# Optimization experiments

Hardware: AMD Instinct MI355X
Metric: run time of the kernel (lower is better)

The kernel has to match this reference:

```python
import jax, jax.numpy as jnp
import numpy as np

IN_FEATS = 64
ONSET = 0.8
CUTOFF = 1.0
N_NODES = 100000
N_EDGES = 1600000


def smooth_cutoff(d):
    # 1 below onset, 0 above cutoff, smooth cosine ramp in between
    x = (d - ONSET) / (CUTOFF - ONSET)
    ramp = 0.5 * (jnp.cos(jnp.pi * jnp.clip(x, 0.0, 1.0)) + 1.0)
    return jnp.where(d <= ONSET, 1.0, jnp.where(d >= CUTOFF, 0.0, ramp))


def setup_inputs() -> dict:
    key = jax.random.key(0)
    ks = jax.random.split(key, 8)
    h = jax.random.normal(ks[0], (N_NODES, IN_FEATS), dtype=jnp.float32)
    dist = jax.random.uniform(ks[1], (N_EDGES,), dtype=jnp.float32)
    W1 = jax.random.normal(ks[2], (IN_FEATS, IN_FEATS), dtype=jnp.float32) / jnp.sqrt(IN_FEATS)
    b1 = jnp.zeros((IN_FEATS,), dtype=jnp.float32)
    W2 = jax.random.normal(ks[3], (IN_FEATS, IN_FEATS), dtype=jnp.float32) / jnp.sqrt(IN_FEATS)
    b2 = jnp.zeros((IN_FEATS,), dtype=jnp.float32)
    src_idx = jax.random.randint(ks[4], (N_EDGES,), 0, N_NODES, dtype=jnp.int64 if jax.config.jax_enable_x64 else jnp.int32).astype(jnp.int32)
    dst_idx = jax.random.randint(ks[5], (N_EDGES,), 0, N_NODES, dtype=jnp.int32)
    return {"h": h, "dist": dist, "W1": W1, "b1": b1, "W2": W2, "b2": b2,
            "src_idx": src_idx, "dst_idx": dst_idx}


def reference(h, dist, W1, b1, W2, b2, src_idx, dst_idx):
    gamma = jnp.float32(IN_FEATS / (CUTOFF - 0.0))  # in_feats / (range hi - lo)
    muk = jnp.linspace(0.0, CUTOFF, IN_FEATS, dtype=jnp.float32)  # [K]
    # per-edge RBF basis: [E, K]
    rbf = jnp.exp(-gamma * (dist[:, None] - muk[None, :]) ** 2)
    fcut = smooth_cutoff(dist)[:, None]  # [E, 1]
    msg = h[src_idx] * rbf * fcut  # gather src feats, [E, K]
    agg = jax.ops.segment_sum(msg, dst_idx, num_segments=N_NODES)  # [N, K]
    # MLP: Linear -> softplus -> Linear
    hid = jax.nn.softplus(agg @ W1 + b1)
    out = hid @ W2 + b2
    return out
```

## Files before the change

kernel.cpp:

```cpp
#include <hip/hip_runtime.h>
#include <hip/hip_fp16.h>
#include <math.h>

#define IN_FEATS 64
#define N_NODES 100000
#define N_EDGES 1600000
#define BSHIFT 7
#define NPB 128
#define NBUCK ((N_NODES + NPB - 1) / NPB)
#define CAP 4088
#define PCHUNK 8192
#define PGRID ((N_EDGES + PCHUNK - 1) / PCHUNK)
#define NGRP (N_NODES / 16)

#define KSCALE 9.6089785f

typedef __attribute__((ext_vector_type(8))) short short8_t;
typedef __attribute__((ext_vector_type(4))) float f32x4_t;

#define MFMA16(a, b, c) __builtin_amdgcn_mfma_f32_16x16x32_bf16(a, b, c, 0, 0, 0)

__device__ __forceinline__ unsigned short bf16_rne(float x) {
    unsigned u = __float_as_uint(x);
    unsigned r = u + 0x7FFFu + ((u >> 16) & 1u);
    return (unsigned short)(r >> 16);
}

__device__ __forceinline__ short8_t u4_to_s8(uint4 v) {
    union { uint4 u; short8_t s; } cv; cv.u = v; return cv.s;
}

__device__ __forceinline__ void split8(float4 a, float4 b,
                                       short8_t* hi, short8_t* lo) {
    short8_t h, l;
#define SP(I, X) { unsigned short hu = bf16_rne(X); \
        float hf = __uint_as_float((unsigned)hu << 16); \
        unsigned short lu = bf16_rne((X) - hf); \
        h[I] = (short)hu; l[I] = (short)lu; }
    SP(0, a.x) SP(1, a.y) SP(2, a.z) SP(3, a.w)
    SP(4, b.x) SP(5, b.y) SP(6, b.z) SP(7, b.w)
#undef SP
    *hi = h; *lo = l;
}

__device__ __forceinline__ float edge_coef(float d, float mu) {
    float t = d - mu;
    float rbf = __expf(-64.0f * t * t);
    float x  = (d - 0.8f) * 5.0f;
    float xc = fminf(fmaxf(x, 0.0f), 1.0f);
    float ramp = 0.5f * (__cosf(3.14159265358979323846f * xc) + 1.0f);
    float fc = (d <= 0.8f) ? 1.0f : ((d >= 1.0f) ? 0.0f : ramp);
    return rbf * fc;
}

__device__ __forceinline__ float cutoff_fc(float d) {
    float x  = (d - 0.8f) * 5.0f;
    float xc = fminf(fmaxf(x, 0.0f), 1.0f);
    float ramp = 0.5f * (__cosf(3.14159265358979323846f * xc) + 1.0f);
    return (d <= 0.8f) ? 1.0f : ((d >= 1.0f) ? 0.0f : ramp);
}

__global__ __launch_bounds__(256) void init_kernel(int* __restrict__ bcursor,
                                                   int* __restrict__ offs,
                                                   const float* __restrict__ W1,
                                                   const float* __restrict__ W2,
                                                   uint4* __restrict__ wfrag,
                                                   const float* __restrict__ h,
                                                   unsigned short* __restrict__ hb) {
    int i = blockIdx.x * 256 + threadIdx.x;
    if (i < NBUCK) bcursor[i] = i * CAP;
    if (i == 0) offs[N_NODES] = N_EDGES;
    if (i < 2048) {
        int lane  = i & 63;
        int tile  = (i >> 6) & 7;
        int hl    = (i >> 9) & 1;
        int layer = (i >> 10) & 1;
        const float* W = layer ? W2 : W1;
        int kbase = (tile >> 2) * 32 + (lane >> 4) * 8;
        int j     = (tile & 3) * 16 + (lane & 15);
        unsigned p[4];
        #pragma unroll
        for (int e = 0; e < 8; e += 2) {
            float x0 = W[(kbase + e) * 64 + j];
            float x1 = W[(kbase + e + 1) * 64 + j];
            unsigned short u0, u1;
            if (hl == 0) {
                u0 = bf16_rne(x0);
                u1 = bf16_rne(x1);
            } else {
                unsigned short h0 = bf16_rne(x0);
                unsigned short h1 = bf16_rne(x1);
                u0 = bf16_rne(x0 - __uint_as_float((unsigned)h0 << 16));
                u1 = bf16_rne(x1 - __uint_as_float((unsigned)h1 << 16));
            }
            p[e >> 1] = (unsigned)u0 | ((unsigned)u1 << 16);
        }
        wfrag[i] = make_uint4(p[0], p[1], p[2], p[3]);
    }
    if (i < N_NODES * 8) {
        const float4* p = (const float4*)(h + (size_t)i * 8);
        float4 a = p[0], b = p[1];
        unsigned u0 = (unsigned)bf16_rne(a.x) | ((unsigned)bf16_rne(a.y) << 16);
        unsigned u1 = (unsigned)bf16_rne(a.z) | ((unsigned)bf16_rne(a.w) << 16);
        unsigned u2 = (unsigned)bf16_rne(b.x) | ((unsigned)bf16_rne(b.y) << 16);
        unsigned u3 = (unsigned)bf16_rne(b.z) | ((unsigned)bf16_rne(b.w) << 16);
        *(uint4*)(hb + (size_t)i * 8) = make_uint4(u0, u1, u2, u3);
    }
}

__global__ __launch_bounds__(1024) void partition_kernel(const int* __restrict__ dst,
                                                         const int* __restrict__ src,
                                                         const float* __restrict__ dist,
                                                         int* __restrict__ bcursor,
                                                         int2* __restrict__ brec) {
    __shared__ int hist[NBUCK];
    __shared__ int base_[NBUCK];
    int tid = threadIdx.x;
    for (int i = tid; i < NBUCK; i += 1024) hist[i] = 0;
    __syncthreads();

    int e0 = blockIdx.x * PCHUNK;
    int e1 = min(e0 + PCHUNK, N_EDGES);

    for (int t = e0 + tid; t < e1; t += 1024)
        atomicAdd(&hist[dst[t] >> BSHIFT], 1);
    __syncthreads();

    for (int i = tid; i < NBUCK; i += 1024) {
        int hv = hist[i];
        if (hv) base_[i] = atomicAdd(&bcursor[i], hv);
        hist[i] = 0;
    }
    __syncthreads();

    for (int t = e0 + tid; t < e1; t += 1024) {
        int d  = dst[t];
        int b  = d >> BSHIFT;
        int r  = atomicAdd(&hist[b], 1);
        float dv = dist[t];
        float fc = cutoff_fc(dv);
        float lfc = (fc > 0.0f) ? __log2f(fc) : -512.0f;
        unsigned dq = (unsigned)(fminf(fmaxf(dv, 0.0f), 1.0f) * 65535.0f + 0.5f);
        unsigned hf = (unsigned)__half_as_ushort(__float2half(lfc));
        int2 rec;
        rec.x = src[t] | ((d & (NPB - 1)) << 17);
        rec.y = (int)((hf << 16) | dq);
        brec[(size_t)base_[b] + r] = rec;
    }
}

__global__ __launch_bounds__(1024) void bscan_kernel(const int* __restrict__ bcursor,
                                                     int* __restrict__ boffs) {
    __shared__ int lds[1024];
    int tid = threadIdx.x;
    int v = (tid < NBUCK) ? (bcursor[tid] - tid * CAP) : 0;
    lds[tid] = v;
    __syncthreads();
    for (int off = 1; off < 1024; off <<= 1) {
        int x = (tid >= off) ? lds[tid - off] : 0;
        __syncthreads();
        lds[tid] += x;
        __syncthreads();
    }
    if (tid < NBUCK) boffs[tid] = lds[tid] - v;
    if (tid == 0) boffs[NBUCK] = N_EDGES;
}

__global__ __launch_bounds__(256) void node_sort_kernel(const int2* __restrict__ brec,
                                                        const int* __restrict__ boffs,
                                                        int2* __restrict__ rec_sorted,
                                                        int* __restrict__ offs) {
    __shared__ int cntL[NPB];
    __shared__ int scanL[NPB];
    __shared__ int curL[NPB];
    __shared__ int2 stage[CAP];

    int b   = blockIdx.x;
    int tid = threadIdx.x;
    int beg = boffs[b];
    int cnt = boffs[b + 1] - beg;
    size_t pbase = (size_t)b * CAP;
    int node0 = b << BSHIFT;

    for (int i = tid; i < NPB; i += 256) cntL[i] = 0;
    __syncthreads();

    for (int t = tid; t < cnt; t += 256) {
        int2 r = brec[pbase + t];
        stage[t] = r;
        atomicAdd(&cntL[(r.x >> 17) & (NPB - 1)], 1);
    }
    __syncthreads();

    if (tid < NPB) scanL[tid] = cntL[tid];
    __syncthreads();
    for (int off = 1; off < NPB; off <<= 1) {
        int x = 0;
        if (tid < NPB && tid >= off) x = scanL[tid - off];
        __syncthreads();
        if (tid < NPB) scanL[tid] += x;
        __syncthreads();
    }
    if (tid < NPB) {
        int excl = scanL[tid] - cntL[tid];
        curL[tid] = excl;
        int node = node0 + tid;
        if (node < N_NODES) offs[node] = beg + excl;
    }
    __syncthreads();

    for (int t = tid; t < cnt; t += 256) {
        int2 r = stage[t];
        int dl = (r.x >> 17) & (NPB - 1);
        int p  = atomicAdd(&curL[dl], 1);
        rec_sorted[(size_t)beg + p] = r;
    }
}

__global__ __launch_bounds__(256) void agg_bf16_kernel(
    const unsigned short* __restrict__ hb,
    const int* __restrict__ offs,
    const int2* __restrict__ rec_sorted,
    float* __restrict__ out)
{
    int w    = threadIdx.x >> 6;
    int lane = threadIdx.x & 63;
    int node = blockIdx.x * 4 + w;
    if (node >= N_NODES) return;

    int beg = __builtin_amdgcn_readfirstlane(offs[node]);
    int end = __builtin_amdgcn_readfirstlane(offs[node + 1]);
    float muK = (float)lane * (KSCALE / 63.0f);
    float acc0 = 0.0f, acc1 = 0.0f;

#define REC(J, ACC) { \
        int2 r_ = rec_sorted[(size_t)(J)]; \
        int rx_ = __builtin_amdgcn_readfirstlane(r_.x); \
        unsigned ry_ = (unsigned)__builtin_amdgcn_readfirstlane(r_.y); \
        unsigned hvu_ = (unsigned)hb[((size_t)(rx_ & 0x1FFFF) << 6) + lane]; \
        float hv_ = __uint_as_float(hvu_ << 16); \
        float dqf_ = (float)(ry_ & 0xFFFFu); \
        float lfc_ = __half2float(__ushort_as_half((unsigned short)(ry_ >> 16))); \
        float t_  = fmaf(dqf_, (KSCALE / 65535.0f), -muK); \
        float a_  = fmaf(-t_, t_, lfc_); \
        ACC = fmaf(hv_, exp2f(a_), ACC); }

    int i = beg;
    int main_end = beg + ((end - beg) & ~7);
    for (; i < main_end; i += 8) {
        REC(i + 0, acc0) REC(i + 1, acc1) REC(i + 2, acc0) REC(i + 3, acc1)
        REC(i + 4, acc0) REC(i + 5, acc1) REC(i + 6, acc0) REC(i + 7, acc1)
    }
    for (; i < end; ++i) { REC(i, acc0) }
#undef REC

    out[(size_t)node * 64 + lane] = acc0 + acc1;
}

__global__ __launch_bounds__(256) void agg_kernel(
    const float* __restrict__ h,
    const int* __restrict__ offs,
    const int2* __restrict__ rec_sorted,
    float* __restrict__ out)
{
    int w    = threadIdx.x >> 6;
    int lane = threadIdx.x & 63;
    int node = blockIdx.x * 4 + w;
    if (node >= N_NODES) return;

    int beg = __builtin_amdgcn_readfirstlane(offs[node]);
    int end = __builtin_amdgcn_readfirstlane(offs[node + 1]);
    float muK = (float)lane * (KSCALE / 63.0f);
    float acc0 = 0.0f, acc1 = 0.0f;

#define REC(J, ACC) { \
        int2 r_ = rec_sorted[(size_t)(J)]; \
        int rx_ = __builtin_amdgcn_readfirstlane(r_.x); \
        unsigned ry_ = (unsigned)__builtin_amdgcn_readfirstlane(r_.y); \
        float hv_ = h[((size_t)(rx_ & 0x1FFFF) << 6) + lane]; \
        float dqf_ = (float)(ry_ & 0xFFFFu); \
        float lfc_ = __half2float(__ushort_as_half((unsigned short)(ry_ >> 16))); \
        float t_  = fmaf(dqf_, (KSCALE / 65535.0f), -muK); \
        float a_  = fmaf(-t_, t_, lfc_); \
        ACC = fmaf(hv_, exp2f(a_), ACC); }

    int i = beg;
    int main_end = beg + ((end - beg) & ~7);
    for (; i < main_end; i += 8) {
        REC(i + 0, acc0) REC(i + 1, acc1) REC(i + 2, acc0) REC(i + 3, acc1)
        REC(i + 4, acc0) REC(i + 5, acc1) REC(i + 6, acc0) REC(i + 7, acc1)
    }
    for (; i < end; ++i) { REC(i, acc0) }
#undef REC

    out[(size_t)node * 64 + lane] = acc0 + acc1;
}

__global__ __launch_bounds__(256) void mlp_kernel(
    float* __restrict__ io, const uint4* __restrict__ wfrag,
    const float* __restrict__ b1, const float* __restrict__ b2)
{
    __shared__ float hidL[4][16][68];

    int tid  = threadIdx.x;
    int lane = tid & 63;
    int wv   = tid >> 6;
    int grp  = blockIdx.x * 4 + wv;
    if (grp >= NGRP) return;
    int node0 = grp * 16;
    int lrow = lane & 15, lk = lane >> 4;

    const float* arow = io + (size_t)(node0 + lrow) * 64 + lk * 8;
    float4 t0 = *(const float4*)(arow);
    float4 t1 = *(const float4*)(arow + 4);
    float4 t2 = *(const float4*)(arow + 32);
    float4 t3 = *(const float4*)(arow + 36);
    short8_t Ah0, Al0, Ah1, Al1;
    split8(t0, t1, &Ah0, &Al0);
    split8(t2, t3, &Ah1, &Al1);

    f32x4_t acc[4];
    #pragma unroll
    for (int n = 0; n < 4; ++n) {
        float b = b1[n * 16 + lrow];
        acc[n] = (f32x4_t){b, b, b, b};
    }
    #pragma unroll
    for (int n = 0; n < 4; ++n) {
        short8_t wh0 = u4_to_s8(wfrag[(n) * 64 + lane]);
        short8_t wh1 = u4_to_s8(wfrag[(4 + n) * 64 + lane]);
        short8_t wl0 = u4_to_s8(wfrag[512 + n * 64 + lane]);
        short8_t wl1 = u4_to_s8(wfrag[512 + (4 + n) * 64 + lane]);
        f32x4_t c = acc[n];
        c = MFMA16(Ah0, wh0, c);
        c = MFMA16(Ah1, wh1, c);
        c = MFMA16(Ah0, wl0, c);
        c = MFMA16(Ah1, wl1, c);
        c = MFMA16(Al0, wh0, c);
        c = MFMA16(Al1, wh1, c);
        acc[n] = c;
    }

    #pragma unroll
    for (int n = 0; n < 4; ++n) {
        #pragma unroll
        for (int r = 0; r < 4; ++r) {
            float v = acc[n][r];
            float e = exp2f(v * 1.44269504089f);
            float sp = 0.69314718056f * __log2f(1.0f + e);
            v = (v > 20.0f) ? v : sp;
            hidL[wv][lk * 4 + r][n * 16 + lrow] = v;
        }
    }
    __threadfence_block();

    const float* hrow = &hidL[wv][lrow][lk * 8];
    float4 h0 = *(const float4*)(hrow);
    float4 h1 = *(const float4*)(hrow + 4);
    float4 h2 = *(const float4*)(hrow + 32);
    float4 h3 = *(const float4*)(hrow + 36);
    short8_t Bh0, Bl0, Bh1, Bl1;
    split8(h0, h1, &Bh0, &Bl0);
    split8(h2, h3, &Bh1, &Bl1);

    f32x4_t oac[4];
    #pragma unroll
    for (int n = 0; n < 4; ++n) {
        float b = b2[n * 16 + lrow];
        oac[n] = (f32x4_t){b, b, b, b};
    }
    #pragma unroll
    for (int n = 0; n < 4; ++n) {
        short8_t wh0 = u4_to_s8(wfrag[1024 + n * 64 + lane]);
        short8_t wh1 = u4_to_s8(wfrag[1024 + (4 + n) * 64 + lane]);
        short8_t wl0 = u4_to_s8(wfrag[1536 + n * 64 + lane]);
        short8_t wl1 = u4_to_s8(wfrag[1536 + (4 + n) * 64 + lane]);
        f32x4_t c = oac[n];
        c = MFMA16(Bh0, wh0, c);
        c = MFMA16(Bh1, wh1, c);
        c = MFMA16(Bh0, wl0, c);
        c = MFMA16(Bh1, wl1, c);
        c = MFMA16(Bl0, wh0, c);
        c = MFMA16(Bl1, wh1, c);
        oac[n] = c;
    }

    #pragma unroll
    for (int n = 0; n < 4; ++n) {
        #pragma unroll
        for (int r = 0; r < 4; ++r) {
            io[(size_t)(node0 + lk * 4 + r) * 64 + n * 16 + lrow] = oac[n][r];
        }
    }
}

__global__ __launch_bounds__(256) void schnet_edge_kernel(
    const float* __restrict__ h,
    const float* __restrict__ dist,
    const int* __restrict__ src_idx,
    const int* __restrict__ dst_idx,
    float* __restrict__ agg)
{
    long long idx = (long long)blockIdx.x * 256 + threadIdx.x;
    int e = (int)(idx >> 6);
    if (e >= N_EDGES) return;
    int k = (int)(idx & 63);
    float d = dist[e];
    float c = edge_coef(d, (float)k * (1.0f / 63.0f));
    int s  = src_idx[e];
    int dn = dst_idx[e];
    atomicAdd(&agg[(long long)dn * 64 + k], h[(long long)s * 64 + k] * c);
}

__global__ __launch_bounds__(256) void mlp_fallback_kernel(
    float* __restrict__ io,
    const float* __restrict__ W1, const float* __restrict__ b1,
    const float* __restrict__ W2, const float* __restrict__ b2)
{
    __shared__ float sW1[64 * 64];
    __shared__ float sW2[64 * 64];
    __shared__ float sRow[4][64];
    __shared__ float sHid[4][64];
    int tid = threadIdx.x;
    for (int i = tid; i < 4096; i += 256) { sW1[i] = W1[i]; sW2[i] = W2[i]; }
    __syncthreads();
    int lane = tid & 63, w = tid >> 6;
    float bb1 = b1[lane], bb2 = b2[lane];
    for (int base = blockIdx.x * 4; base < N_NODES; base += gridDim.x * 4) {
        int node = base + w;
        if (node < N_NODES) sRow[w][lane] = io[(size_t)node * 64 + lane];
        __syncthreads();
        float a = bb1;
        #pragma unroll
        for (int k = 0; k < 64; ++k) a = fmaf(sRow[w][k], sW1[k * 64 + lane], a);
        sHid[w][lane] = (a > 20.f) ? a : log1pf(__expf(a));
        __syncthreads();
        float c = bb2;
        #pragma unroll
        for (int k = 0; k < 64; ++k) c = fmaf(sHid[w][k], sW2[k * 64 + lane], c);
        if (node < N_NODES) io[(size_t)node * 64 + lane] = c;
        __syncthreads();
    }
}

extern "C" void kernel_launch(void* const* d_in, const int* in_sizes, int n_in,
                              void* d_out, int out_size, void* d_ws, size_t ws_size,
                              hipStream_t stream) {
    const float* h    = (const float*)d_in[0];
    const float* dist = (const float*)d_in[1];
    const float* W1   = (const float*)d_in[2];
    const float* b1   = (const float*)d_in[3];
    const float* W2   = (const float*)d_in[4];
    const float* b2   = (const float*)d_in[5];
    const int* src    = (const int*)d_in[6];
    const int* dst    = (const int*)d_in[7];
    float* out        = (float*)d_out;

    const size_t WFRAG_B = 32768;
    const size_t HB_B    = (size_t)N_NODES * 64 * 2;
    const size_t RS_B    = (size_t)N_EDGES * 8;
    const size_t INTS_B  = ((size_t)NBUCK + 1 + NBUCK + N_NODES + 1) * 4;
    size_t need_f32  = WFRAG_B + RS_B + INTS_B;
    size_t need_bf16 = WFRAG_B + HB_B + RS_B + INTS_B;

    if (ws_size >= need_f32) {
        bool use_bf16 = (ws_size >= need_bf16);
        char* p = (char*)d_ws;
        uint4* wfrag = (uint4*)p;              p += WFRAG_B;
        unsigned short* hb = (unsigned short*)p;
        if (use_bf16)                          p += HB_B;
        int2* rec_sorted = (int2*)p;           p += RS_B;
        int* boffs   = (int*)p;
        int* bcursor = boffs + NBUCK + 1;
        int* offs    = bcursor + NBUCK;

        int2* brec = (int2*)d_out;

        int init_grid = use_bf16 ? (N_NODES * 8 + 255) / 256 : 16;
        init_kernel<<<init_grid, 256, 0, stream>>>(bcursor, offs, W1, W2, wfrag,
                                                   h, use_bf16 ? hb : nullptr);
        partition_kernel<<<PGRID, 1024, 0, stream>>>(dst, src, dist, bcursor, brec);
        bscan_kernel<<<1, 1024, 0, stream>>>(bcursor, boffs);
        node_sort_kernel<<<NBUCK, 256, 0, stream>>>(brec, boffs, rec_sorted, offs);
        if (use_bf16)
            agg_bf16_kernel<<<N_NODES / 4, 256, 0, stream>>>(hb, offs, rec_sorted, out);
        else
            agg_kernel<<<N_NODES / 4, 256, 0, stream>>>(h, offs, rec_sorted, out);
        mlp_kernel<<<(NGRP + 3) / 4, 256, 0, stream>>>(out, wfrag, b1, b2);
    } else {
        hipMemsetAsync(out, 0, (size_t)N_NODES * IN_FEATS * sizeof(float), stream);
        long long total = (long long)N_EDGES * 64;
        schnet_edge_kernel<<<(int)((total + 255) / 256), 256, 0, stream>>>(
            h, dist, src, dst, out);
        mlp_fallback_kernel<<<2048, 256, 0, stream>>>(out, W1, b1, W2, b2);
    }
}
```

Measured before the change: 116.8 us.

## Fuse h bf16 conversion into partition kernel and drop bucket-scan kernel

Moves the h-to-bf16 conversion out of init_kernel into extra blocks of the partition kernel, so init becomes a tiny 16-block launch. The separate bucket prefix-scan kernel is removed, and each node_sort block instead recomputes its start offset by reducing the preceding bucket counts. The partition loop also caches dst, src and dist in registers so each edge is loaded once instead of twice. Together these cut one launch and kernel boundaries, at the cost of redundant O(NBUCK) reduction work in every sort block.

```diff
diff --git a/kernel.cpp b/kernel.cpp
--- a/kernel.cpp
+++ b/kernel.cpp
@@ -11,7 +11,9 @@
 #define CAP 4088
 #define PCHUNK 8192
 #define PGRID ((N_EDGES + PCHUNK - 1) / PCHUNK)
+#define HBLK ((N_NODES * 8 + 1023) / 1024)
 #define NGRP (N_NODES / 16)
+#define EPT (PCHUNK / 1024)
 
 #define KSCALE 9.6089785f
 
@@ -64,9 +66,7 @@
                                                    int* __restrict__ offs,
                                                    const float* __restrict__ W1,
                                                    const float* __restrict__ W2,
-                                                   uint4* __restrict__ wfrag,
-                                                   const float* __restrict__ h,
-                                                   unsigned short* __restrict__ hb) {
+                                                   uint4* __restrict__ wfrag) {
     int i = blockIdx.x * 256 + threadIdx.x;
     if (i < NBUCK) bcursor[i] = i * CAP;
     if (i == 0) offs[N_NODES] = N_EDGES;
@@ -97,33 +97,59 @@
         }
         wfrag[i] = make_uint4(p[0], p[1], p[2], p[3]);
     }
-    if (i < N_NODES * 8) {
-        const float4* p = (const float4*)(h + (size_t)i * 8);
-        float4 a = p[0], b = p[1];
-        unsigned u0 = (unsigned)bf16_rne(a.x) | ((unsigned)bf16_rne(a.y) << 16);
-        unsigned u1 = (unsigned)bf16_rne(a.z) | ((unsigned)bf16_rne(a.w) << 16);
-        unsigned u2 = (unsigned)bf16_rne(b.x) | ((unsigned)bf16_rne(b.y) << 16);
-        unsigned u3 = (unsigned)bf16_rne(b.z) | ((unsigned)bf16_rne(b.w) << 16);
-        *(uint4*)(hb + (size_t)i * 8) = make_uint4(u0, u1, u2, u3);
-    }
-}
-
-__global__ __launch_bounds__(1024) void partition_kernel(const int* __restrict__ dst,
-                                                         const int* __restrict__ src,
-                                                         const float* __restrict__ dist,
-                                                         int* __restrict__ bcursor,
-                                                         int2* __restrict__ brec) {
+}
+
+__global__ __launch_bounds__(1024) void part_conv_kernel(
+    const int* __restrict__ dst,
+    const int* __restrict__ src,
+    const float* __restrict__ dist,
+    int* __restrict__ bcursor,
+    int2* __restrict__ brec,
+    const float* __restrict__ h,
+    unsigned short* __restrict__ hb)
+{
     __shared__ int hist[NBUCK];
     __shared__ int base_[NBUCK];
+
+    int bid = blockIdx.x;
     int tid = threadIdx.x;
+
+    if (bid >= PGRID) {
+        if (hb != nullptr) {
+            int idx = (bid - PGRID) * 1024 + tid;
+            if (idx < N_NODES * 8) {
+                const float4* p = (const float4*)(h + (size_t)idx * 8);
+                float4 a = p[0], b = p[1];
+                unsigned u0 = (unsigned)bf16_rne(a.x) | ((unsigned)bf16_rne(a.y) << 16);
+                unsigned u1 = (unsigned)bf16_rne(a.z) | ((unsigned)bf16_rne(a.w) << 16);
+                unsigned u2 = (unsigned)bf16_rne(b.x) | ((unsigned)bf16_rne(b.y) << 16);
+                unsigned u3 = (unsigned)bf16_rne(b.z) | ((unsigned)bf16_rne(b.w) << 16);
+                *(uint4*)(hb + (size_t)idx * 8) = make_uint4(u0, u1, u2, u3);
+            }
+        }
+        return;
+    }
+
     for (int i = tid; i < NBUCK; i += 1024) hist[i] = 0;
     __syncthreads();
 
-    int e0 = blockIdx.x * PCHUNK;
-    int e1 = min(e0 + PCHUNK, N_EDGES);
-
-    for (int t = e0 + tid; t < e1; t += 1024)
-        atomicAdd(&hist[dst[t] >> BSHIFT], 1);
+    int e0  = bid * PCHUNK;
+    int rem = N_EDGES - e0;
+
+    int   dcache[EPT];
+    int   scache[EPT];
+    float vcache[EPT];
+    #pragma unroll
+    for (int u = 0; u < EPT; ++u) {
+        int t = tid + u * 1024;
+        bool v = t < rem;
+        int tt = v ? (e0 + t) : e0;
+        dcache[u] = dst[tt];
+        scache[u] = src[tt];
+        vcache[u] = dist[tt];
+        if (v) atomicAdd(&hist[dcache[u] >> BSHIFT], 1);
+        else   dcache[u] = -1;
+    }
     __syncthreads();
 
     for (int i = tid; i < NBUCK; i += 1024) {
@@ -133,52 +159,48 @@
     }
     __syncthreads();
 
-    for (int t = e0 + tid; t < e1; t += 1024) {
-        int d  = dst[t];
-        int b  = d >> BSHIFT;
-        int r  = atomicAdd(&hist[b], 1);
-        float dv = dist[t];
-        float fc = cutoff_fc(dv);
-        float lfc = (fc > 0.0f) ? __log2f(fc) : -512.0f;
-        unsigned dq = (unsigned)(fminf(fmaxf(dv, 0.0f), 1.0f) * 65535.0f + 0.5f);
-        unsigned hf = (unsigned)__half_as_ushort(__float2half(lfc));
-        int2 rec;
-        rec.x = src[t] | ((d & (NPB - 1)) << 17);
-        rec.y = (int)((hf << 16) | dq);
-        brec[(size_t)base_[b] + r] = rec;
-    }
-}
-
-__global__ __launch_bounds__(1024) void bscan_kernel(const int* __restrict__ bcursor,
-                                                     int* __restrict__ boffs) {
-    __shared__ int lds[1024];
-    int tid = threadIdx.x;
-    int v = (tid < NBUCK) ? (bcursor[tid] - tid * CAP) : 0;
-    lds[tid] = v;
-    __syncthreads();
-    for (int off = 1; off < 1024; off <<= 1) {
-        int x = (tid >= off) ? lds[tid - off] : 0;
-        __syncthreads();
-        lds[tid] += x;
-        __syncthreads();
-    }
-    if (tid < NBUCK) boffs[tid] = lds[tid] - v;
-    if (tid == 0) boffs[NBUCK] = N_EDGES;
+    #pragma unroll
+    for (int u = 0; u < EPT; ++u) {
+        int d = dcache[u];
+        if (d >= 0) {
+            int bkt = d >> BSHIFT;
+            int r   = atomicAdd(&hist[bkt], 1);
+            float dv = vcache[u];
+            float fc = cutoff_fc(dv);
+            float lfc = (fc > 0.0f) ? __log2f(fc) : -512.0f;
+            unsigned dq = (unsigned)(fminf(fmaxf(dv, 0.0f), 1.0f) * 65535.0f + 0.5f);
+            unsigned hf = (unsigned)__half_as_ushort(__float2half(lfc));
+            int2 rec;
+            rec.x = scache[u] | ((d & (NPB - 1)) << 17);
+            rec.y = (int)((hf << 16) | dq);
+            brec[(size_t)base_[bkt] + r] = rec;
+        }
+    }
 }
 
 __global__ __launch_bounds__(256) void node_sort_kernel(const int2* __restrict__ brec,
-                                                        const int* __restrict__ boffs,
+                                                        const int* __restrict__ bcursor,
                                                         int2* __restrict__ rec_sorted,
                                                         int* __restrict__ offs) {
     __shared__ int cntL[NPB];
     __shared__ int scanL[NPB];
     __shared__ int curL[NPB];
+    __shared__ int red[256];
     __shared__ int2 stage[CAP];
 
     int b   = blockIdx.x;
     int tid = threadIdx.x;
-    int beg = boffs[b];
-    int cnt = boffs[b + 1] - beg;
+
+    int s = 0;
+    for (int i = tid; i < b; i += 256) s += bcursor[i] - i * CAP;
+    red[tid] = s;
+    __syncthreads();
+    for (int off = 128; off > 0; off >>= 1) {
+        if (tid < off) red[tid] += red[tid + off];
+        __syncthreads();
+    }
+    int beg = red[0];
+    int cnt = bcursor[b] - b * CAP;
     size_t pbase = (size_t)b * CAP;
     int node0 = b << BSHIFT;
 
@@ -459,7 +481,7 @@
     const size_t WFRAG_B = 32768;
     const size_t HB_B    = (size_t)N_NODES * 64 * 2;
     const size_t RS_B    = (size_t)N_EDGES * 8;
-    const size_t INTS_B  = ((size_t)NBUCK + 1 + NBUCK + N_NODES + 1) * 4;
+    const size_t INTS_B  = ((size_t)NBUCK + N_NODES + 1) * 4;
     size_t need_f32  = WFRAG_B + RS_B + INTS_B;
     size_t need_bf16 = WFRAG_B + HB_B + RS_B + INTS_B;
 
@@ -470,18 +492,16 @@
         unsigned short* hb = (unsigned short*)p;
         if (use_bf16)                          p += HB_B;
         int2* rec_sorted = (int2*)p;           p += RS_B;
-        int* boffs   = (int*)p;
-        int* bcursor = boffs + NBUCK + 1;
+        int* bcursor = (int*)p;
         int* offs    = bcursor + NBUCK;
 
         int2* brec = (int2*)d_out;
 
-        int init_grid = use_bf16 ? (N_NODES * 8 + 255) / 256 : 16;
-        init_kernel<<<init_grid, 256, 0, stream>>>(bcursor, offs, W1, W2, wfrag,
-                                                   h, use_bf16 ? hb : nullptr);
-        partition_kernel<<<PGRID, 1024, 0, stream>>>(dst, src, dist, bcursor, brec);
-        bscan_kernel<<<1, 1024, 0, stream>>>(bcursor, boffs);
-        node_sort_kernel<<<NBUCK, 256, 0, stream>>>(brec, boffs, rec_sorted, offs);
+        init_kernel<<<16, 256, 0, stream>>>(bcursor, offs, W1, W2, wfrag);
+        int pcgrid = use_bf16 ? (PGRID + HBLK) : PGRID;
+        part_conv_kernel<<<pcgrid, 1024, 0, stream>>>(dst, src, dist, bcursor, brec,
+                                                      h, use_bf16 ? hb : nullptr);
+        node_sort_kernel<<<NBUCK, 256, 0, stream>>>(brec, bcursor, rec_sorted, offs);
         if (use_bf16)
             agg_bf16_kernel<<<N_NODES / 4, 256, 0, stream>>>(hb, offs, rec_sorted, out);
         else
```

After: 112.6 us (median of 2 runs). -3.6%, faster.
